# Performance work log

Measured on AMD Instinct MI355X. Metric: run time of the kernel, lower is better.

The kernel has to match this reference:

```python
import jax, jax.numpy as jnp
import numpy as np

H = 8
D_MODEL = 512
NEG = -1e9  # fp32 masking value from the torch source


def setup_inputs() -> dict:
    key = jax.random.key(0)
    ks = jax.random.split(key, 13)
    B, T, C, D = 2, 512, 8, D_MODEL
    s = 1.0 / np.sqrt(D)
    inp = {
        "query": jax.random.normal(ks[0], (B, T, C, D), jnp.float32),
        "key": jax.random.normal(ks[1], (B, T, C, D), jnp.float32),
        "value": jax.random.normal(ks[2], (B, T, C, D), jnp.float32),
        "mask": jax.random.randint(ks[3], (B, T, T, 1), 0, 2, jnp.int32),
        # four Linear(d_model, d_model) layers, stored as (in, out)
        "Wq": jax.random.normal(ks[4], (D, D), jnp.float32) * s,
        "bq": jax.random.normal(ks[5], (D,), jnp.float32) * s,
        "Wk": jax.random.normal(ks[6], (D, D), jnp.float32) * s,
        "bk": jax.random.normal(ks[7], (D,), jnp.float32) * s,
        "Wv": jax.random.normal(ks[8], (D, D), jnp.float32) * s,
        "bv": jax.random.normal(ks[9], (D,), jnp.float32) * s,
        "Wo": jax.random.normal(ks[10], (D, D), jnp.float32) * s,
        "bo": jax.random.normal(ks[11], (D,), jnp.float32) * s,
    }
    return inp


def _mha(query, key, value, mask, Wq, bq, Wk, bk, Wv, bv, Wo, bo):
    B, T, C, D = query.shape
    h, dk = H, D // H

    def proj(x, W, b):
        y = (x @ W + b).reshape(B, T, C, h, dk)
        return jnp.transpose(y, (0, 3, 2, 1, 4))  # [B,h,C,T,dk] (torch transpose(1,3))

    q = proj(query, Wq, bq)
    k = proj(key, Wk, bk)
    v = proj(value, Wv, bv)

    scores = jnp.einsum("bhctd,bhcsd->bhcts", q, k) / np.sqrt(dk)  # [B,h,C,T,T]
    # The torch view/transpose/view dance is just a permutation putting C last;
    # it is equivalent to masking scores[b,h,c,t,s] where mask[b,t,s,0]==0
    # (mask broadcast over heads h and channels c).
    m = mask[:, :, :, 0]  # [B,T,Tk]
    scores = jnp.where(m[:, None, None, :, :] == 0, NEG, scores)
    p_attn = jax.nn.softmax(scores, axis=-1)
    # dropout omitted (inference/deterministic reference)
    x = jnp.einsum("bhcts,bhcsd->bhctd", p_attn, v)  # [B,h,C,T,dk]
    x = jnp.transpose(x, (0, 3, 2, 1, 4)).reshape(B, T, C, D)
    return x @ Wo + bo


def reference(query, key, value, mask, Wq, bq, Wk, bk, Wv, bv, Wo, bo):
    return _mha(query, key, value, mask, Wq, bq, Wk, bk, Wv, bv, Wo, bo)
```

## Files before the change

### kernel.cpp

```cpp
#include <hip/hip_runtime.h>
#include <hip/hip_bf16.h>

typedef __bf16 bf16;
typedef __bf16 bf16x8 __attribute__((ext_vector_type(8)));
typedef float floatx4 __attribute__((ext_vector_type(4)));


union Pack8 { bf16 h[8]; uint4 u; };
union Pack4 { bf16 h[4]; unsigned long long u; };

__device__ __forceinline__ void store_pack8(bf16* dst, float4 a, float4 b) {
    Pack8 p;
    p.h[0] = (bf16)a.x; p.h[1] = (bf16)a.y; p.h[2] = (bf16)a.z; p.h[3] = (bf16)a.w;
    p.h[4] = (bf16)b.x; p.h[5] = (bf16)b.y; p.h[6] = (bf16)b.z; p.h[7] = (bf16)b.w;
    *(uint4*)dst = p.u;
}

#define BAR_LG asm volatile("s_waitcnt lgkmcnt(0)\n\ts_barrier" ::: "memory")

__global__ __launch_bounds__(256) void wtr_kernel(
    const float* __restrict__ Wq, const float* __restrict__ Wk,
    const float* __restrict__ Wv, const float* __restrict__ Wo,
    bf16* __restrict__ WT)
{
    __shared__ float Ts[64][65];
    const int tid = threadIdx.x;
    const int k0 = blockIdx.x * 64;
    const int n0 = blockIdx.y * 64;
    const int z  = blockIdx.z;
    const float* W = (z == 0) ? Wq : (z == 1) ? Wk : (z == 2) ? Wv : Wo;
    bf16* O = WT + (size_t)z * 512 * 512;
    #pragma unroll
    for (int i = 0; i < 16; i++) {
        const int r = i * 4 + (tid >> 6), c = tid & 63;
        Ts[r][c] = W[(size_t)(k0 + r) * 512 + n0 + c];
    }
    __syncthreads();
    #pragma unroll
    for (int i = 0; i < 16; i++) {
        const int a = i * 4 + (tid >> 6), c = tid & 63;
        O[(size_t)(n0 + a) * 512 + k0 + c] = (bf16)Ts[c][a];
    }
}

__global__ __launch_bounds__(512, 4) void gemm_qkv(
    const float* __restrict__ Aq, const float* __restrict__ Ak,
    const float* __restrict__ Av, const bf16* __restrict__ WT,
    const float* __restrict__ Bq, const float* __restrict__ Bk,
    const float* __restrict__ Bv,
    bf16* __restrict__ Oq, bf16* __restrict__ Ok, bf16* __restrict__ Ov)
{
    __shared__ __align__(16) bf16 smem[17408];
    bf16* Ab0 = smem;
    bf16* Ab1 = smem + 4096;
    bf16* Bb0 = smem + 8192;
    bf16* Bb1 = smem + 12288;

    const int z = blockIdx.z;
    const float* A    = (z == 0) ? Aq : (z == 1) ? Ak : Av;
    const float* bias = (z == 0) ? Bq : (z == 1) ? Bk : Bv;
    bf16* out         = (z == 0) ? Oq : (z == 1) ? Ok : Ov;
    const bf16* BT = WT + (size_t)z * 262144;
    const float scale = (z == 0) ? 0.125f : 1.0f;

    const int tid  = threadIdx.x;
    const int lane = tid & 63;
    const int wave = tid >> 6;
    const int quad = lane >> 4;
    const int l16  = lane & 15;
    const int mblk = blockIdx.x * 128;
    const int nblk = blockIdx.y * 128;

    const int srow = wave * 16 + (lane >> 2);
    const int scol = (lane & 3) * 8;
    const float* Ag = A + (size_t)(mblk + srow) * 512 + scol;
    const bf16* Bg  = BT + (size_t)(nblk + srow) * 512 + scol;
    const int aoff = srow * 32 + scol;

    const int wr = (wave >> 1) * 32;
    const int wc = (wave & 1) * 64;

    floatx4 acc[2][4] = {};

    float4 ax0 = *(const float4*)(Ag);
    float4 ax1 = *(const float4*)(Ag + 4);
    uint4  bx  = *(const uint4*)(Bg);
    store_pack8(Ab0 + aoff, ax0, ax1);
    *(uint4*)(Bb0 + aoff) = bx;
    float4 ay0 = *(const float4*)(Ag + 32);
    float4 ay1 = *(const float4*)(Ag + 36);
    uint4  by  = *(const uint4*)(Bg + 32);
    store_pack8(Ab1 + aoff, ay0, ay1);
    *(uint4*)(Bb1 + aoff) = by;
    ax0 = *(const float4*)(Ag + 64);
    ax1 = *(const float4*)(Ag + 68);
    bx  = *(const uint4*)(Bg + 64);
    BAR_LG;

    #pragma unroll
    for (int t = 0; t < 16; t++) {
        bf16* Ab = (t & 1) ? Ab1 : Ab0;
        bf16* Bb = (t & 1) ? Bb1 : Bb0;
        bf16x8 a[2], b[4];
        #pragma unroll
        for (int mt = 0; mt < 2; mt++)
            a[mt] = *(const bf16x8*)(Ab + (wr + mt * 16 + l16) * 32 + quad * 8);
        #pragma unroll
        for (int nt = 0; nt < 4; nt++)
            b[nt] = *(const bf16x8*)(Bb + (wc + nt * 16 + l16) * 32 + quad * 8);
        #pragma unroll
        for (int mt = 0; mt < 2; mt++)
            #pragma unroll
            for (int nt = 0; nt < 4; nt++)
                acc[mt][nt] = __builtin_amdgcn_mfma_f32_16x16x32_bf16(
                    a[mt], b[nt], acc[mt][nt], 0, 0, 0);
        if (t <= 12) {
            const int kL = (t + 3) * 32;
            if (t & 1) {
                ax0 = *(const float4*)(Ag + kL);
                ax1 = *(const float4*)(Ag + kL + 4);
                bx  = *(const uint4*)(Bg + kL);
            } else {
                ay0 = *(const float4*)(Ag + kL);
                ay1 = *(const float4*)(Ag + kL + 4);
                by  = *(const uint4*)(Bg + kL);
            }
        }
        if (t <= 13) {
            BAR_LG;
            if (t & 1) {
                store_pack8(Ab + aoff, ay0, ay1);
                *(uint4*)(Bb + aoff) = by;
            } else {
                store_pack8(Ab + aoff, ax0, ax1);
                *(uint4*)(Bb + aoff) = bx;
            }
            BAR_LG;
        }
    }

    if (z != 2) {
        #pragma unroll
        for (int mt = 0; mt < 2; mt++) {
            #pragma unroll
            for (int nt = 0; nt < 4; nt++) {
                const int colg = nblk + wc + nt * 16 + l16;
                const float bb = bias[colg];
                #pragma unroll
                for (int r = 0; r < 4; r++) {
                    const int rowg = mblk + wr + mt * 16 + quad * 4 + r;
                    const float v = (acc[mt][nt][r] + bb) * scale;
                    const int b_ = rowg >> 12;
                    const int t_ = (rowg >> 3) & 511;
                    const int c  = rowg & 7;
                    const int h  = colg >> 6;
                    const int d  = colg & 63;
                    const int hd = b_ * 64 + h * 8 + c;
                    out[((size_t)hd * 512 + t_) * 64 + d] = (bf16)v;
                }
            }
        }
    } else {
        __syncthreads();
        typedef bf16 TsmRow[136];
        TsmRow* Tsm = (TsmRow*)smem;
        #pragma unroll
        for (int mt = 0; mt < 2; mt++) {
            #pragma unroll
            for (int nt = 0; nt < 4; nt++) {
                const int cl = wc + nt * 16 + l16;
                const float bb = bias[nblk + cl];
                #pragma unroll
                for (int r = 0; r < 4; r++)
                    Tsm[wr + mt * 16 + quad * 4 + r][cl] =
                        (bf16)(acc[mt][nt][r] + bb);
            }
        }
        __syncthreads();
        const int b_ = mblk >> 12;
        const int t0 = (mblk >> 3) & 511;
        #pragma unroll
        for (int ch = tid; ch < 1024; ch += 512) {
            const int col = ch >> 3, c = ch & 7;
            const int h = (nblk + col) >> 6, d = (nblk + col) & 63;
            const int hd = b_ * 64 + h * 8 + c;
            Pack8 lo, hi;
            #pragma unroll
            for (int j = 0; j < 8; j++) lo.h[j] = Tsm[j * 8 + c][col];
            #pragma unroll
            for (int j = 0; j < 8; j++) hi.h[j] = Tsm[(j + 8) * 8 + c][col];
            bf16* dst = out + ((size_t)hd * 64 + d) * 512 + t0;
            *(uint4*)dst = lo.u;
            *(uint4*)(dst + 8) = hi.u;
        }
    }
}

__global__ __launch_bounds__(512, 4) void gemm_o(
    const bf16* __restrict__ A, const bf16* __restrict__ BT,
    const float* __restrict__ bias, float* __restrict__ out)
{
    __shared__ __align__(16) bf16 smem[16384];
    bf16* Ab0 = smem;
    bf16* Ab1 = smem + 4096;
    bf16* Bb0 = smem + 8192;
    bf16* Bb1 = smem + 12288;

    const int tid  = threadIdx.x;
    const int lane = tid & 63;
    const int wave = tid >> 6;
    const int quad = lane >> 4;
    const int l16  = lane & 15;
    const int mblk = blockIdx.x * 128;
    const int nblk = blockIdx.y * 128;

    const int srow = wave * 16 + (lane >> 2);
    const int scol = (lane & 3) * 8;
    const bf16* Ag = A + (size_t)(mblk + srow) * 512 + scol;
    const bf16* Bg = BT + (size_t)(nblk + srow) * 512 + scol;
    const int aoff = srow * 32 + scol;

    const int wr = (wave >> 1) * 32;
    const int wc = (wave & 1) * 64;

    floatx4 acc[2][4] = {};

    uint4 xa = *(const uint4*)(Ag);
    uint4 xb = *(const uint4*)(Bg);
    *(uint4*)(Ab0 + aoff) = xa;
    *(uint4*)(Bb0 + aoff) = xb;
    uint4 ya = *(const uint4*)(Ag + 32);
    uint4 yb = *(const uint4*)(Bg + 32);
    *(uint4*)(Ab1 + aoff) = ya;
    *(uint4*)(Bb1 + aoff) = yb;
    xa = *(const uint4*)(Ag + 64);
    xb = *(const uint4*)(Bg + 64);
    BAR_LG;

    #pragma unroll
    for (int t = 0; t < 16; t++) {
        bf16* Ab = (t & 1) ? Ab1 : Ab0;
        bf16* Bb = (t & 1) ? Bb1 : Bb0;
        bf16x8 a[2], b[4];
        #pragma unroll
        for (int mt = 0; mt < 2; mt++)
            a[mt] = *(const bf16x8*)(Ab + (wr + mt * 16 + l16) * 32 + quad * 8);
        #pragma unroll
        for (int nt = 0; nt < 4; nt++)
            b[nt] = *(const bf16x8*)(Bb + (wc + nt * 16 + l16) * 32 + quad * 8);
        #pragma unroll
        for (int mt = 0; mt < 2; mt++)
            #pragma unroll
            for (int nt = 0; nt < 4; nt++)
                acc[mt][nt] = __builtin_amdgcn_mfma_f32_16x16x32_bf16(
                    a[mt], b[nt], acc[mt][nt], 0, 0, 0);
        if (t <= 12) {
            const int kL = (t + 3) * 32;
            if (t & 1) { xa = *(const uint4*)(Ag + kL); xb = *(const uint4*)(Bg + kL); }
            else       { ya = *(const uint4*)(Ag + kL); yb = *(const uint4*)(Bg + kL); }
        }
        if (t <= 13) {
            BAR_LG;
            if (t & 1) { *(uint4*)(Ab + aoff) = ya; *(uint4*)(Bb + aoff) = yb; }
            else       { *(uint4*)(Ab + aoff) = xa; *(uint4*)(Bb + aoff) = xb; }
            BAR_LG;
        }
    }

    #pragma unroll
    for (int mt = 0; mt < 2; mt++) {
        #pragma unroll
        for (int nt = 0; nt < 4; nt++) {
            const int colg = nblk + wc + nt * 16 + l16;
            const float bb = bias[colg];
            #pragma unroll
            for (int r = 0; r < 4; r++) {
                const int rowg = mblk + wr + mt * 16 + quad * 4 + r;
                out[(size_t)rowg * 512 + colg] = acc[mt][nt][r] + bb;
            }
        }
    }
}

#define PST 520

__global__ __launch_bounds__(256, 2) void attn_kernel(
    const bf16* __restrict__ Qws, const bf16* __restrict__ Kws,
    const bf16* __restrict__ Vtws, const int* __restrict__ mask,
    bf16* __restrict__ Xws)
{
    __shared__ bf16 Psm[64][PST];
    __shared__ float redM[4][64];
    __shared__ float redS[4][64];
    const int tid  = threadIdx.x;
    const int wave = tid >> 6;
    const int lane = tid & 63;
    const int quad = lane >> 4;
    const int l16  = lane & 15;
    const int s_ = blockIdx.x;
    const int o_ = ((s_ & 7) << 7) | (s_ >> 3);
    const int hd = o_ >> 3;
    const int qt = o_ & 7;
    const int q0 = qt * 64;
    const int b = hd >> 6;
    const int h = (hd >> 3) & 7;
    const int c = hd & 7;

    const bf16* Qh = Qws + (size_t)hd * 512 * 64;
    const bf16* Kh = Kws + (size_t)hd * 512 * 64;
    const int* mp = mask + ((size_t)b * 512 + q0) * 512;

    bf16x8 aq[4][2];
    #pragma unroll
    for (int s = 0; s < 4; s++) {
        aq[s][0] = *(const bf16x8*)(Qh + (size_t)(q0 + s * 16 + l16) * 64 + quad * 8);
        aq[s][1] = *(const bf16x8*)(Qh + (size_t)(q0 + s * 16 + l16) * 64 + 32 + quad * 8);
    }

    floatx4 sv[4][8];
    #pragma unroll
    for (int s = 0; s < 4; s++)
        #pragma unroll
        for (int nt = 0; nt < 8; nt++)
            sv[s][nt] = (floatx4){0.f, 0.f, 0.f, 0.f};

    #pragma unroll
    for (int nt = 0; nt < 8; nt++) {
        const int s0 = wave * 128 + nt * 16;
        bf16x8 bk0 = *(const bf16x8*)(Kh + (size_t)(s0 + l16) * 64 + quad * 8);
        bf16x8 bk1 = *(const bf16x8*)(Kh + (size_t)(s0 + l16) * 64 + 32 + quad * 8);
        #pragma unroll
        for (int s = 0; s < 4; s++) {
            sv[s][nt] = __builtin_amdgcn_mfma_f32_16x16x32_bf16(
                bk0, aq[s][0], sv[s][nt], 0, 0, 0);
            sv[s][nt] = __builtin_amdgcn_mfma_f32_16x16x32_bf16(
                bk1, aq[s][1], sv[s][nt], 0, 0, 0);
        }
    }

    float mx[4] = {-3.0e38f, -3.0e38f, -3.0e38f, -3.0e38f};
    #pragma unroll
    for (int s = 0; s < 4; s++)
        #pragma unroll
        for (int nt = 0; nt < 8; nt++) {
            const int4 mv = *(const int4*)(
                mp + (size_t)(s * 16 + l16) * 512 + wave * 128 + nt * 16 + quad * 4);
            float v0 = sv[s][nt][0] + ((mv.x == 0) ? -1.0e9f : 0.0f);
            float v1 = sv[s][nt][1] + ((mv.y == 0) ? -1.0e9f : 0.0f);
            float v2 = sv[s][nt][2] + ((mv.z == 0) ? -1.0e9f : 0.0f);
            float v3 = sv[s][nt][3] + ((mv.w == 0) ? -1.0e9f : 0.0f);
            sv[s][nt][0] = v0; sv[s][nt][1] = v1;
            sv[s][nt][2] = v2; sv[s][nt][3] = v3;
            mx[s] = fmaxf(mx[s], fmaxf(fmaxf(v0, v1), fmaxf(v2, v3)));
        }
    #pragma unroll
    for (int s = 0; s < 4; s++) {
        mx[s] = fmaxf(mx[s], __shfl_xor(mx[s], 16, 64));
        mx[s] = fmaxf(mx[s], __shfl_xor(mx[s], 32, 64));
    }
    if (quad == 0)
        #pragma unroll
        for (int s = 0; s < 4; s++) redM[wave][s * 16 + l16] = mx[s];
    __syncthreads();

    float mf[4], sum[4] = {0.f, 0.f, 0.f, 0.f};
    #pragma unroll
    for (int s = 0; s < 4; s++) {
        const int qr = s * 16 + l16;
        mf[s] = fmaxf(fmaxf(redM[0][qr], redM[1][qr]),
                      fmaxf(redM[2][qr], redM[3][qr]));
    }
    #pragma unroll
    for (int s = 0; s < 4; s++)
        #pragma unroll
        for (int nt = 0; nt < 8; nt++)
            #pragma unroll
            for (int r = 0; r < 4; r++) {
                const float e = __expf(sv[s][nt][r] - mf[s]);
                sv[s][nt][r] = e;
                sum[s] += e;
            }
    #pragma unroll
    for (int s = 0; s < 4; s++) {
        sum[s] += __shfl_xor(sum[s], 16, 64);
        sum[s] += __shfl_xor(sum[s], 32, 64);
    }
    if (quad == 0)
        #pragma unroll
        for (int s = 0; s < 4; s++) redS[wave][s * 16 + l16] = sum[s];
    __syncthreads();

    float inv[4];
    #pragma unroll
    for (int s = 0; s < 4; s++) {
        const int qr = s * 16 + l16;
        inv[s] = 1.f / (redS[0][qr] + redS[1][qr] + redS[2][qr] + redS[3][qr]);
    }
    #pragma unroll
    for (int s = 0; s < 4; s++)
        #pragma unroll
        for (int nt = 0; nt < 8; nt++) {
            Pack4 pk;
            #pragma unroll
            for (int r = 0; r < 4; r++)
                pk.h[r] = (bf16)(sv[s][nt][r] * inv[s]);
            *(unsigned long long*)&Psm[s * 16 + l16][wave * 128 + nt * 16 + quad * 4]
                = pk.u;
        }
    __syncthreads();

    const bf16* Vh = Vtws + (size_t)hd * 64 * 512;
    const int d0 = wave * 16;
    floatx4 o[4] = {};
    #pragma unroll
    for (int ks = 0; ks < 16; ks++) {
        bf16x8 bv = *(const bf16x8*)(Vh + (size_t)(d0 + l16) * 512 + ks * 32 + quad * 8);
        #pragma unroll
        for (int rt = 0; rt < 4; rt++) {
            bf16x8 ap = *(const bf16x8*)(&Psm[rt * 16 + l16][ks * 32 + quad * 8]);
            o[rt] = __builtin_amdgcn_mfma_f32_16x16x32_bf16(ap, bv, o[rt], 0, 0, 0);
        }
    }
    #pragma unroll
    for (int rt = 0; rt < 4; rt++)
        #pragma unroll
        for (int r = 0; r < 4; r++) {
            const int q = q0 + rt * 16 + quad * 4 + r;
            const size_t row = ((size_t)b * 512 + q) * 8 + c;
            Xws[row * 512 + h * 64 + d0 + l16] = (bf16)o[rt][r];
        }
}

extern "C" void kernel_launch(void* const* d_in, const int* in_sizes, int n_in,
                              void* d_out, int out_size, void* d_ws, size_t ws_size,
                              hipStream_t stream)
{
    const float* qin  = (const float*)d_in[0];
    const float* kin  = (const float*)d_in[1];
    const float* vin  = (const float*)d_in[2];
    const int*   mask = (const int*)d_in[3];
    const float* Bq = (const float*)d_in[5];
    const float* Bk = (const float*)d_in[7];
    const float* Bv = (const float*)d_in[9];
    const float* Bo = (const float*)d_in[11];
    float* out = (float*)d_out;

    const size_t R = (size_t)8192 * 512;
    bf16* r0 = (bf16*)d_ws;
    bf16* r1 = r0 + R;
    bf16* r2 = r1 + R;
    bf16* r3 = r2 + R;
    bf16* WT = r3 + R;

    wtr_kernel<<<dim3(8, 8, 4), dim3(256), 0, stream>>>(
        (const float*)d_in[4], (const float*)d_in[6],
        (const float*)d_in[8], (const float*)d_in[10], WT);
    gemm_qkv<<<dim3(64, 4, 3), dim3(512), 0, stream>>>(
        qin, kin, vin, WT, Bq, Bk, Bv, r0, r1, r2);
    attn_kernel<<<dim3(1024), dim3(256), 0, stream>>>(
        r0, r1, r2, mask, r3);
    gemm_o<<<dim3(64, 4), dim3(512), 0, stream>>>(
        r3, WT + (size_t)3 * 262144, Bo, out);
}
```

Before: 195.4 us.

## Retile QKV GEMM to full-width 64x512 tiles and drop redundant barrier

The QKV projection GEMM now has each block compute a 64-row by 512-column tile, so every fp32 activation row is loaded and converted to bf16 once instead of once per 128-column block. LDS grows to hold the wider B tiles, occupancy is lowered to two blocks per CU, and the grid shrinks to 384 blocks. The V transpose epilogue is reworked into four staged column chunks to fit shared memory. Separately, the second barrier after the LDS stores in each k-iteration is removed in both GEMMs, relying on double buffering for safety. Costs are more registers per thread, fewer resident blocks, and extra barriers in the V epilogue.

```diff
diff --git a/kernel.cpp b/kernel.cpp
--- a/kernel.cpp
+++ b/kernel.cpp
@@ -8,12 +8,19 @@
 
 union Pack8 { bf16 h[8]; uint4 u; };
 union Pack4 { bf16 h[4]; unsigned long long u; };
+union Pack4f { bf16 h[4]; unsigned long long u; };
 
 __device__ __forceinline__ void store_pack8(bf16* dst, float4 a, float4 b) {
     Pack8 p;
     p.h[0] = (bf16)a.x; p.h[1] = (bf16)a.y; p.h[2] = (bf16)a.z; p.h[3] = (bf16)a.w;
     p.h[4] = (bf16)b.x; p.h[5] = (bf16)b.y; p.h[6] = (bf16)b.z; p.h[7] = (bf16)b.w;
     *(uint4*)dst = p.u;
+}
+
+__device__ __forceinline__ void store_pack4(bf16* dst, float4 a) {
+    Pack4f p;
+    p.h[0] = (bf16)a.x; p.h[1] = (bf16)a.y; p.h[2] = (bf16)a.z; p.h[3] = (bf16)a.w;
+    *(unsigned long long*)dst = p.u;
 }
 
 #define BAR_LG asm volatile("s_waitcnt lgkmcnt(0)\n\ts_barrier" ::: "memory")
@@ -43,18 +50,18 @@
     }
 }
 
-__global__ __launch_bounds__(512, 4) void gemm_qkv(
+__global__ __launch_bounds__(512, 2) void gemm_qkv(
     const float* __restrict__ Aq, const float* __restrict__ Ak,
     const float* __restrict__ Av, const bf16* __restrict__ WT,
     const float* __restrict__ Bq, const float* __restrict__ Bk,
     const float* __restrict__ Bv,
     bf16* __restrict__ Oq, bf16* __restrict__ Ok, bf16* __restrict__ Ov)
 {
-    __shared__ __align__(16) bf16 smem[17408];
+    __shared__ __align__(16) bf16 smem[36864];
     bf16* Ab0 = smem;
-    bf16* Ab1 = smem + 4096;
-    bf16* Bb0 = smem + 8192;
-    bf16* Bb1 = smem + 12288;
+    bf16* Ab1 = smem + 2048;
+    bf16* Bb0 = smem + 4096;
+    bf16* Bb1 = smem + 20480;
 
     const int z = blockIdx.z;
     const float* A    = (z == 0) ? Aq : (z == 1) ? Ak : Av;
@@ -68,48 +75,58 @@
     const int wave = tid >> 6;
     const int quad = lane >> 4;
     const int l16  = lane & 15;
-    const int mblk = blockIdx.x * 128;
-    const int nblk = blockIdx.y * 128;
-
-    const int srow = wave * 16 + (lane >> 2);
-    const int scol = (lane & 3) * 8;
-    const float* Ag = A + (size_t)(mblk + srow) * 512 + scol;
-    const bf16* Bg  = BT + (size_t)(nblk + srow) * 512 + scol;
-    const int aoff = srow * 32 + scol;
-
-    const int wr = (wave >> 1) * 32;
-    const int wc = (wave & 1) * 64;
-
-    floatx4 acc[2][4] = {};
-
-    float4 ax0 = *(const float4*)(Ag);
-    float4 ax1 = *(const float4*)(Ag + 4);
-    uint4  bx  = *(const uint4*)(Bg);
-    store_pack8(Ab0 + aoff, ax0, ax1);
-    *(uint4*)(Bb0 + aoff) = bx;
-    float4 ay0 = *(const float4*)(Ag + 32);
-    float4 ay1 = *(const float4*)(Ag + 36);
-    uint4  by  = *(const uint4*)(Bg + 32);
-    store_pack8(Ab1 + aoff, ay0, ay1);
-    *(uint4*)(Bb1 + aoff) = by;
-    ax0 = *(const float4*)(Ag + 64);
-    ax1 = *(const float4*)(Ag + 68);
-    bx  = *(const uint4*)(Bg + 64);
+    const int mblk = blockIdx.x * 64;
+
+    const int arow = tid >> 3;
+    const int acol = (tid & 7) * 4;
+    const float* Ag = A + (size_t)(mblk + arow) * 512 + acol;
+    const int aoff = arow * 32 + acol;
+    const int brow = tid >> 2;
+    const int bcol = (tid & 3) * 8;
+    const bf16* Bg = BT + (size_t)brow * 512 + bcol;
+    const int boff = brow * 32 + bcol;
+
+    const int wc = wave * 64;
+
+    floatx4 acc[4][4] = {};
+
+    float4 ax; uint4 bx[4];
+    float4 ay; uint4 by[4];
+    ax = *(const float4*)(Ag);
+    #pragma unroll
+    for (int i = 0; i < 4; i++)
+        bx[i] = *(const uint4*)(Bg + (size_t)i * 128 * 512);
+    store_pack4(Ab0 + aoff, ax);
+    #pragma unroll
+    for (int i = 0; i < 4; i++)
+        *(uint4*)(Bb0 + i * 128 * 32 + boff) = bx[i];
+    ay = *(const float4*)(Ag + 32);
+    #pragma unroll
+    for (int i = 0; i < 4; i++)
+        by[i] = *(const uint4*)(Bg + (size_t)i * 128 * 512 + 32);
+    store_pack4(Ab1 + aoff, ay);
+    #pragma unroll
+    for (int i = 0; i < 4; i++)
+        *(uint4*)(Bb1 + i * 128 * 32 + boff) = by[i];
+    ax = *(const float4*)(Ag + 64);
+    #pragma unroll
+    for (int i = 0; i < 4; i++)
+        bx[i] = *(const uint4*)(Bg + (size_t)i * 128 * 512 + 64);
     BAR_LG;
 
     #pragma unroll
     for (int t = 0; t < 16; t++) {
         bf16* Ab = (t & 1) ? Ab1 : Ab0;
         bf16* Bb = (t & 1) ? Bb1 : Bb0;
-        bf16x8 a[2], b[4];
-        #pragma unroll
-        for (int mt = 0; mt < 2; mt++)
-            a[mt] = *(const bf16x8*)(Ab + (wr + mt * 16 + l16) * 32 + quad * 8);
+        bf16x8 a[4], b[4];
+        #pragma unroll
+        for (int mt = 0; mt < 4; mt++)
+            a[mt] = *(const bf16x8*)(Ab + (mt * 16 + l16) * 32 + quad * 8);
         #pragma unroll
         for (int nt = 0; nt < 4; nt++)
             b[nt] = *(const bf16x8*)(Bb + (wc + nt * 16 + l16) * 32 + quad * 8);
         #pragma unroll
-        for (int mt = 0; mt < 2; mt++)
+        for (int mt = 0; mt < 4; mt++)
             #pragma unroll
             for (int nt = 0; nt < 4; nt++)
                 acc[mt][nt] = __builtin_amdgcn_mfma_f32_16x16x32_bf16(
@@ -117,38 +134,43 @@
         if (t <= 12) {
             const int kL = (t + 3) * 32;
             if (t & 1) {
-                ax0 = *(const float4*)(Ag + kL);
-                ax1 = *(const float4*)(Ag + kL + 4);
-                bx  = *(const uint4*)(Bg + kL);
+                ax = *(const float4*)(Ag + kL);
+                #pragma unroll
+                for (int i = 0; i < 4; i++)
+                    bx[i] = *(const uint4*)(Bg + (size_t)i * 128 * 512 + kL);
             } else {
-                ay0 = *(const float4*)(Ag + kL);
-                ay1 = *(const float4*)(Ag + kL + 4);
-                by  = *(const uint4*)(Bg + kL);
-            }
-        }
+                ay = *(const float4*)(Ag + kL);
+                #pragma unroll
+                for (int i = 0; i < 4; i++)
+                    by[i] = *(const uint4*)(Bg + (size_t)i * 128 * 512 + kL);
+            }
+        }
+        BAR_LG;
         if (t <= 13) {
-            BAR_LG;
             if (t & 1) {
-                store_pack8(Ab + aoff, ay0, ay1);
-                *(uint4*)(Bb + aoff) = by;
+                store_pack4(Ab + aoff, ay);
+                #pragma unroll
+                for (int i = 0; i < 4; i++)
+                    *(uint4*)(Bb + i * 128 * 32 + boff) = by[i];
             } else {
-                store_pack8(Ab + aoff, ax0, ax1);
-                *(uint4*)(Bb + aoff) = bx;
-            }
-            BAR_LG;
+                store_pack4(Ab + aoff, ax);
+                #pragma unroll
+                for (int i = 0; i < 4; i++)
+                    *(uint4*)(Bb + i * 128 * 32 + boff) = bx[i];
+            }
         }
     }
 
     if (z != 2) {
         #pragma unroll
-        for (int mt = 0; mt < 2; mt++) {
+        for (int mt = 0; mt < 4; mt++) {
             #pragma unroll
             for (int nt = 0; nt < 4; nt++) {
-                const int colg = nblk + wc + nt * 16 + l16;
+                const int colg = wc + nt * 16 + l16;
                 const float bb = bias[colg];
                 #pragma unroll
                 for (int r = 0; r < 4; r++) {
-                    const int rowg = mblk + wr + mt * 16 + quad * 4 + r;
+                    const int rowg = mblk + mt * 16 + quad * 4 + r;
                     const float v = (acc[mt][nt][r] + bb) * scale;
                     const int b_ = rowg >> 12;
                     const int t_ = (rowg >> 3) & 511;
@@ -164,34 +186,38 @@
         __syncthreads();
         typedef bf16 TsmRow[136];
         TsmRow* Tsm = (TsmRow*)smem;
-        #pragma unroll
-        for (int mt = 0; mt < 2; mt++) {
-            #pragma unroll
-            for (int nt = 0; nt < 4; nt++) {
-                const int cl = wc + nt * 16 + l16;
-                const float bb = bias[nblk + cl];
-                #pragma unroll
-                for (int r = 0; r < 4; r++)
-                    Tsm[wr + mt * 16 + quad * 4 + r][cl] =
-                        (bf16)(acc[mt][nt][r] + bb);
-            }
-        }
-        __syncthreads();
         const int b_ = mblk >> 12;
         const int t0 = (mblk >> 3) & 511;
         #pragma unroll
-        for (int ch = tid; ch < 1024; ch += 512) {
-            const int col = ch >> 3, c = ch & 7;
-            const int h = (nblk + col) >> 6, d = (nblk + col) & 63;
-            const int hd = b_ * 64 + h * 8 + c;
-            Pack8 lo, hi;
-            #pragma unroll
-            for (int j = 0; j < 8; j++) lo.h[j] = Tsm[j * 8 + c][col];
-            #pragma unroll
-            for (int j = 0; j < 8; j++) hi.h[j] = Tsm[(j + 8) * 8 + c][col];
-            bf16* dst = out + ((size_t)hd * 64 + d) * 512 + t0;
-            *(uint4*)dst = lo.u;
-            *(uint4*)(dst + 8) = hi.u;
+        for (int cb = 0; cb < 4; cb++) {
+            if ((wave >> 1) == cb) {
+                #pragma unroll
+                for (int mt = 0; mt < 4; mt++) {
+                    #pragma unroll
+                    for (int nt = 0; nt < 4; nt++) {
+                        const int colg = wc + nt * 16 + l16;
+                        const int cl = colg - cb * 128;
+                        const float bb = bias[colg];
+                        #pragma unroll
+                        for (int r = 0; r < 4; r++)
+                            Tsm[mt * 16 + quad * 4 + r][cl] =
+                                (bf16)(acc[mt][nt][r] + bb);
+                    }
+                }
+            }
+            __syncthreads();
+            #pragma unroll
+            for (int e = tid; e < 1024; e += 512) {
+                const int col = e >> 3, c = e & 7;
+                const int gcol = cb * 128 + col;
+                const int h = gcol >> 6, d = gcol & 63;
+                const int hd = b_ * 64 + h * 8 + c;
+                Pack8 pk;
+                #pragma unroll
+                for (int j = 0; j < 8; j++) pk.h[j] = Tsm[j * 8 + c][col];
+                *(uint4*)(out + ((size_t)hd * 64 + d) * 512 + t0) = pk.u;
+            }
+            __syncthreads();
         }
     }
 }
@@ -259,11 +285,10 @@
             if (t & 1) { xa = *(const uint4*)(Ag + kL); xb = *(const uint4*)(Bg + kL); }
             else       { ya = *(const uint4*)(Ag + kL); yb = *(const uint4*)(Bg + kL); }
         }
+        BAR_LG;
         if (t <= 13) {
-            BAR_LG;
             if (t & 1) { *(uint4*)(Ab + aoff) = ya; *(uint4*)(Bb + aoff) = yb; }
             else       { *(uint4*)(Ab + aoff) = xa; *(uint4*)(Bb + aoff) = xb; }
-            BAR_LG;
         }
     }
 
@@ -455,7 +480,7 @@
     wtr_kernel<<<dim3(8, 8, 4), dim3(256), 0, stream>>>(
         (const float*)d_in[4], (const float*)d_in[6],
         (const float*)d_in[8], (const float*)d_in[10], WT);
-    gemm_qkv<<<dim3(64, 4, 3), dim3(512), 0, stream>>>(
+    gemm_qkv<<<dim3(128, 1, 3), dim3(512), 0, stream>>>(
         qin, kin, vin, WT, Bq, Bk, Bv, r0, r1, r2);
     attn_kernel<<<dim3(1024), dim3(256), 0, stream>>>(
         r0, r1, r2, mask, r3);
```

Result: slower. 274.4 us (+40.5%).

## Widen QKV GEMM tile to 128x256 with direct global-to-LDS B loads

Applied to the files above, without the earlier changes.

The QKV projection GEMM now computes a 128x256 output tile per block with 4x4 MFMA accumulators per wave and half as many column blocks. This halves how often the fp32 activations are re-read from global memory. The weight tiles are loaded straight into LDS with global_load_lds, while the activation tile is converted and stored synchronously. This drops the previous register double-buffered prefetch, adds two block barriers per k-step, and lowers the occupancy hint to 3. The V-transpose epilogue is split into two 128-column passes, and gemm_o's double-buffered loop drops to one barrier per iteration.

```diff
diff --git a/kernel.cpp b/kernel.cpp
--- a/kernel.cpp
+++ b/kernel.cpp
@@ -5,6 +5,14 @@
 typedef __bf16 bf16x8 __attribute__((ext_vector_type(8)));
 typedef float floatx4 __attribute__((ext_vector_type(4)));
 
+
+#define AS1 __attribute__((address_space(1)))
+#define AS3 __attribute__((address_space(3)))
+
+__device__ __forceinline__ void gload_lds16(const bf16* g, bf16* l) {
+    __builtin_amdgcn_global_load_lds((const AS1 unsigned int*)g,
+                                     (AS3 unsigned int*)l, 16, 0, 0);
+}
 
 union Pack8 { bf16 h[8]; uint4 u; };
 union Pack4 { bf16 h[4]; unsigned long long u; };
@@ -43,7 +51,7 @@
     }
 }
 
-__global__ __launch_bounds__(512, 4) void gemm_qkv(
+__global__ __launch_bounds__(512, 3) void gemm_qkv(
     const float* __restrict__ Aq, const float* __restrict__ Ak,
     const float* __restrict__ Av, const bf16* __restrict__ WT,
     const float* __restrict__ Bq, const float* __restrict__ Bk,
@@ -51,10 +59,8 @@
     bf16* __restrict__ Oq, bf16* __restrict__ Ok, bf16* __restrict__ Ov)
 {
     __shared__ __align__(16) bf16 smem[17408];
-    bf16* Ab0 = smem;
-    bf16* Ab1 = smem + 4096;
-    bf16* Bb0 = smem + 8192;
-    bf16* Bb1 = smem + 12288;
+    bf16* Asm = smem;
+    bf16* Bsm = smem + 4096;
 
     const int z = blockIdx.z;
     const float* A    = (z == 0) ? Aq : (z == 1) ? Ak : Av;
@@ -69,79 +75,49 @@
     const int quad = lane >> 4;
     const int l16  = lane & 15;
     const int mblk = blockIdx.x * 128;
-    const int nblk = blockIdx.y * 128;
-
-    const int srow = wave * 16 + (lane >> 2);
-    const int scol = (lane & 3) * 8;
-    const float* Ag = A + (size_t)(mblk + srow) * 512 + scol;
-    const bf16* Bg  = BT + (size_t)(nblk + srow) * 512 + scol;
-    const int aoff = srow * 32 + scol;
-
-    const int wr = (wave >> 1) * 32;
-    const int wc = (wave & 1) * 64;
-
-    floatx4 acc[2][4] = {};
-
-    float4 ax0 = *(const float4*)(Ag);
-    float4 ax1 = *(const float4*)(Ag + 4);
-    uint4  bx  = *(const uint4*)(Bg);
-    store_pack8(Ab0 + aoff, ax0, ax1);
-    *(uint4*)(Bb0 + aoff) = bx;
-    float4 ay0 = *(const float4*)(Ag + 32);
-    float4 ay1 = *(const float4*)(Ag + 36);
-    uint4  by  = *(const uint4*)(Bg + 32);
-    store_pack8(Ab1 + aoff, ay0, ay1);
-    *(uint4*)(Bb1 + aoff) = by;
-    ax0 = *(const float4*)(Ag + 64);
-    ax1 = *(const float4*)(Ag + 68);
-    bx  = *(const uint4*)(Bg + 64);
-    BAR_LG;
-
-    #pragma unroll
-    for (int t = 0; t < 16; t++) {
-        bf16* Ab = (t & 1) ? Ab1 : Ab0;
-        bf16* Bb = (t & 1) ? Bb1 : Bb0;
-        bf16x8 a[2], b[4];
-        #pragma unroll
-        for (int mt = 0; mt < 2; mt++)
-            a[mt] = *(const bf16x8*)(Ab + (wr + mt * 16 + l16) * 32 + quad * 8);
+    const int nblk = blockIdx.y * 256;
+
+    const int srowA = tid >> 2;
+    const int scolA = (tid & 3) * 8;
+    const float* Ag = A + (size_t)(mblk + srowA) * 512 + scolA;
+    const int aoff = srowA * 32 + scolA;
+    const int srowB = wave * 16 + (lane >> 2);
+    const int scolB = (lane & 3) * 8;
+    const bf16* Bg0 = BT + (size_t)(nblk + srowB) * 512 + scolB;
+    const bf16* Bg1 = Bg0 + (size_t)128 * 512;
+    bf16* Bl0 = Bsm + wave * 16 * 32;
+    bf16* Bl1 = Bsm + (128 + wave * 16) * 32;
+
+    const int wr = (wave >> 2) * 64;
+    const int wc = (wave & 3) * 64;
+
+    floatx4 acc[4][4] = {};
+    for (int k0 = 0; k0 < 512; k0 += 32) {
+        gload_lds16(Bg0 + k0, Bl0);
+        gload_lds16(Bg1 + k0, Bl1);
+        float4 x0 = *(const float4*)(Ag + k0);
+        float4 x1 = *(const float4*)(Ag + k0 + 4);
+        store_pack8(Asm + aoff, x0, x1);
+        __syncthreads();
+        bf16x8 a[4], b[4];
+        #pragma unroll
+        for (int mt = 0; mt < 4; mt++)
+            a[mt] = *(const bf16x8*)(Asm + (wr + mt * 16 + l16) * 32 + quad * 8);
         #pragma unroll
         for (int nt = 0; nt < 4; nt++)
-            b[nt] = *(const bf16x8*)(Bb + (wc + nt * 16 + l16) * 32 + quad * 8);
-        #pragma unroll
-        for (int mt = 0; mt < 2; mt++)
+            b[nt] = *(const bf16x8*)(Bsm + (wc + nt * 16 + l16) * 32 + quad * 8);
+        #pragma unroll
+        for (int mt = 0; mt < 4; mt++)
             #pragma unroll
             for (int nt = 0; nt < 4; nt++)
                 acc[mt][nt] = __builtin_amdgcn_mfma_f32_16x16x32_bf16(
                     a[mt], b[nt], acc[mt][nt], 0, 0, 0);
-        if (t <= 12) {
-            const int kL = (t + 3) * 32;
-            if (t & 1) {
-                ax0 = *(const float4*)(Ag + kL);
-                ax1 = *(const float4*)(Ag + kL + 4);
-                bx  = *(const uint4*)(Bg + kL);
-            } else {
-                ay0 = *(const float4*)(Ag + kL);
-                ay1 = *(const float4*)(Ag + kL + 4);
-                by  = *(const uint4*)(Bg + kL);
-            }
-        }
-        if (t <= 13) {
-            BAR_LG;
-            if (t & 1) {
-                store_pack8(Ab + aoff, ay0, ay1);
-                *(uint4*)(Bb + aoff) = by;
-            } else {
-                store_pack8(Ab + aoff, ax0, ax1);
-                *(uint4*)(Bb + aoff) = bx;
-            }
-            BAR_LG;
-        }
+        __syncthreads();
     }
 
     if (z != 2) {
         #pragma unroll
-        for (int mt = 0; mt < 2; mt++) {
+        for (int mt = 0; mt < 4; mt++) {
             #pragma unroll
             for (int nt = 0; nt < 4; nt++) {
                 const int colg = nblk + wc + nt * 16 + l16;
@@ -161,37 +137,44 @@
             }
         }
     } else {
-        __syncthreads();
         typedef bf16 TsmRow[136];
         TsmRow* Tsm = (TsmRow*)smem;
-        #pragma unroll
-        for (int mt = 0; mt < 2; mt++) {
-            #pragma unroll
-            for (int nt = 0; nt < 4; nt++) {
-                const int cl = wc + nt * 16 + l16;
-                const float bb = bias[nblk + cl];
-                #pragma unroll
-                for (int r = 0; r < 4; r++)
-                    Tsm[wr + mt * 16 + quad * 4 + r][cl] =
-                        (bf16)(acc[mt][nt][r] + bb);
-            }
-        }
-        __syncthreads();
         const int b_ = mblk >> 12;
         const int t0 = (mblk >> 3) & 511;
         #pragma unroll
-        for (int ch = tid; ch < 1024; ch += 512) {
-            const int col = ch >> 3, c = ch & 7;
-            const int h = (nblk + col) >> 6, d = (nblk + col) & 63;
-            const int hd = b_ * 64 + h * 8 + c;
-            Pack8 lo, hi;
-            #pragma unroll
-            for (int j = 0; j < 8; j++) lo.h[j] = Tsm[j * 8 + c][col];
-            #pragma unroll
-            for (int j = 0; j < 8; j++) hi.h[j] = Tsm[(j + 8) * 8 + c][col];
-            bf16* dst = out + ((size_t)hd * 64 + d) * 512 + t0;
-            *(uint4*)dst = lo.u;
-            *(uint4*)(dst + 8) = hi.u;
+        for (int cb = 0; cb < 2; cb++) {
+            if (((wave & 3) >> 1) == cb) {
+                #pragma unroll
+                for (int mt = 0; mt < 4; mt++) {
+                    #pragma unroll
+                    for (int nt = 0; nt < 4; nt++) {
+                        const int clg = wc + nt * 16 + l16;
+                        const float bb = bias[nblk + clg];
+                        const int cl = clg - cb * 128;
+                        #pragma unroll
+                        for (int r = 0; r < 4; r++)
+                            Tsm[wr + mt * 16 + quad * 4 + r][cl] =
+                                (bf16)(acc[mt][nt][r] + bb);
+                    }
+                }
+            }
+            __syncthreads();
+            #pragma unroll
+            for (int e = tid; e < 1024; e += 512) {
+                const int col = e >> 3, c = e & 7;
+                const int gcol = nblk + cb * 128 + col;
+                const int h = gcol >> 6, d = gcol & 63;
+                const int hd = b_ * 64 + h * 8 + c;
+                Pack8 lo, hi;
+                #pragma unroll
+                for (int j = 0; j < 8; j++) lo.h[j] = Tsm[j * 8 + c][col];
+                #pragma unroll
+                for (int j = 0; j < 8; j++) hi.h[j] = Tsm[(j + 8) * 8 + c][col];
+                bf16* dst = out + ((size_t)hd * 64 + d) * 512 + t0;
+                *(uint4*)dst = lo.u;
+                *(uint4*)(dst + 8) = hi.u;
+            }
+            __syncthreads();
         }
     }
 }
@@ -259,11 +242,10 @@
             if (t & 1) { xa = *(const uint4*)(Ag + kL); xb = *(const uint4*)(Bg + kL); }
             else       { ya = *(const uint4*)(Ag + kL); yb = *(const uint4*)(Bg + kL); }
         }
+        BAR_LG;
         if (t <= 13) {
-            BAR_LG;
             if (t & 1) { *(uint4*)(Ab + aoff) = ya; *(uint4*)(Bb + aoff) = yb; }
             else       { *(uint4*)(Ab + aoff) = xa; *(uint4*)(Bb + aoff) = xb; }
-            BAR_LG;
         }
     }
 
@@ -455,7 +437,7 @@
     wtr_kernel<<<dim3(8, 8, 4), dim3(256), 0, stream>>>(
         (const float*)d_in[4], (const float*)d_in[6],
         (const float*)d_in[8], (const float*)d_in[10], WT);
-    gemm_qkv<<<dim3(64, 4, 3), dim3(512), 0, stream>>>(
+    gemm_qkv<<<dim3(64, 2, 3), dim3(512), 0, stream>>>(
         qin, kin, vin, WT, Bq, Bk, Bv, r0, r1, r2);
     attn_kernel<<<dim3(1024), dim3(256), 0, stream>>>(
         r0, r1, r2, mask, r3);
```

Measured after the change: 190.4 us. 2.6% less time.
